# Performance work log

Hardware: AMD Instinct MI355X
Metric: run time of the kernel (lower is better)

## Reference

```python
import jax, jax.numpy as jnp
import numpy as np

E = 256        # HP.EMBED_SIZE
R = 8          # number of derivation rules / MLPs
S = 512        # number of sequential derivation steps
N = 256        # nodes produced per step
N_INIT = 1024  # initial axiom (thax) embeddings
TOTAL = N_INIT + S * N  # 132096 rows in the vectors buffer
M = 65536      # masked nodes fed to eval_net


def setup_inputs() -> dict:
    key = jax.random.key(0)
    ks = jax.random.split(key, 12)
    rng = np.random.default_rng(0)

    init_vecs = jax.random.normal(ks[0], (N_INIT, E), jnp.float32)
    # rule MLPs: concat(2 parents) -> E (relu) -> E
    W1 = jax.random.normal(ks[1], (R, 2 * E, E), jnp.float32) * (1.0 / np.sqrt(2 * E))
    b1 = jnp.zeros((R, E), jnp.float32)
    W2 = jax.random.normal(ks[2], (R, E, E), jnp.float32) * (1.0 / np.sqrt(E))
    b2 = jnp.zeros((R, E), jnp.float32)
    # eval net: E -> E (relu) -> 1
    eval_W1 = jax.random.normal(ks[3], (E, E), jnp.float32) * (1.0 / np.sqrt(E))
    eval_b1 = jnp.zeros((E,), jnp.float32)
    eval_W2 = jax.random.normal(ks[4], (E, 1), jnp.float32) * (1.0 / np.sqrt(E))
    eval_b2 = jnp.zeros((1,), jnp.float32)

    # step s writes rows [N_INIT + s*N, N_INIT + (s+1)*N)
    ind_steps = (N_INIT + np.arange(S * N, dtype=np.int32)).reshape(S, N)
    # parents drawn causally from already-computed prefix [0, N_INIT + s*N)
    highs = (N_INIT + np.arange(S, dtype=np.int64) * N)[:, None, None]
    pars_ind_steps = (rng.random((S, N, 2)) * highs).astype(np.int32)
    rule_steps = rng.integers(0, R, size=(S,)).astype(np.int32)
    mask = rng.integers(0, TOTAL, size=(M,)).astype(np.int32)

    pos = jax.random.uniform(ks[5], (M,), jnp.float32)
    neg = jax.random.uniform(ks[6], (M,), jnp.float32)
    target = jnp.round(jax.random.uniform(ks[7], (M,), jnp.float32))

    return {
        'init_vecs': init_vecs, 'W1': W1, 'b1': b1, 'W2': W2, 'b2': b2,
        'eval_W1': eval_W1, 'eval_b1': eval_b1, 'eval_W2': eval_W2, 'eval_b2': eval_b2,
        'pos': pos, 'neg': neg, 'target': target,
        'ind_steps': jnp.asarray(ind_steps), 'pars_ind_steps': jnp.asarray(pars_ind_steps),
        'rule_steps': jnp.asarray(rule_steps), 'mask': jnp.asarray(mask),
    }


def reference(init_vecs, W1, b1, W2, b2, eval_W1, eval_b1, eval_W2, eval_b2,
              pos, neg, target, ind_steps, pars_ind_steps, rule_steps, mask):
    vectors = jnp.zeros((TOTAL, E), init_vecs.dtype).at[:N_INIT].set(init_vecs)

    def step(vec, xs):
        inds, pars, r = xs            # [N], [N,2], scalar rule id
        p = vec[pars].reshape(N, 2 * E)   # gather parents
        h = jax.nn.relu(p @ W1[r] + b1[r])
        out = h @ W2[r] + b2[r]
        return vec.at[inds].set(out), None  # scatter new node embeddings

    vectors, _ = jax.lax.scan(step, vectors, (ind_steps, pars_ind_steps, rule_steps))

    x = vectors[mask]
    val = (jax.nn.relu(x @ eval_W1 + eval_b1) @ eval_W2 + eval_b2)[:, 0]

    # pos_weight = POS_WEIGHT_EXTRA * tot_neg / tot_pos (constant w.r.t. grads)
    pw = jax.lax.stop_gradient(jnp.sum(neg) / jnp.maximum(jnp.sum(pos), 1.0))
    # BCEWithLogitsLoss(pos_weight, reduction='none')
    contrib = pw * target * jax.nn.softplus(-val) + (1.0 - target) * jax.nn.softplus(val)
    loss = jnp.sum((pos + neg) * contrib)
    posOK = jnp.sum(pos * (val >= 0))
    negOK = jnp.sum(neg * (val < 0))
    return loss, posOK, negOK
```

## Files before the change

kernel.cpp:

```cpp
#include <hip/hip_runtime.h>
#include <math.h>

#define EMB   256
#define TWOE  512
#define NINIT 1024
#define NSTEP 512
#define NPS   256
#define TOTAL (NINIT + NSTEP * NPS)
#define MM    65536
#define NNODE (NSTEP * NPS)
#define NKEY  2048
#define BTH   512
#define TROWS 32
#define CHK_SH  16384
#define RULE_SH (24 * CHK_SH)

typedef short s16x8 __attribute__((ext_vector_type(8)));
typedef float f32x4 __attribute__((ext_vector_type(4)));

#define OFF_VECH   0ull
#define OFF_VECL   ((size_t)TOTAL * EMB * 2)
#define OFF_VAL    (2ull * (size_t)TOTAL * EMB * 2)
#define OFF_CNT    (OFF_VAL + (size_t)MM * 4)
#define OFF_ACC    (OFF_CNT + 4096)
#define OFF_PW     (OFF_ACC + 64)
#define OFF_KCNT   (OFF_PW + 192)
#define OFF_KOFS   (OFF_KCNT + (size_t)NKEY * 4)
#define OFF_NL     (OFF_KOFS + (size_t)NKEY * 4)
#define OFF_BROWS  (OFF_NL + 256)
#define OFF_LVL8   (OFF_BROWS + (size_t)NNODE * 4)
#define OFF_WSPLIT (OFF_LVL8 + 132352)


__device__ __forceinline__ void store_dev_u32(unsigned* p, unsigned v) {
  asm volatile("global_store_dword %0, %1, off sc0 sc1" :: "v"(p), "v"(v) : "memory");
}
__device__ __forceinline__ void store_dev_b64(void* p, uint2 v) {
  asm volatile("global_store_dwordx2 %0, %1, off sc0 sc1" :: "v"(p), "v"(v) : "memory");
}
__device__ __forceinline__ void store_dev_b128(void* p, uint4 v) {
  store_dev_b64(p, make_uint2(v.x, v.y));
  store_dev_b64((char*)p + 8, make_uint2(v.z, v.w));
}
__device__ __forceinline__ unsigned load_dev_u32(const unsigned* p) {
  unsigned r;
  asm volatile("global_load_dword %0, %1, off sc0 sc1\n\ts_waitcnt vmcnt(0)"
               : "=v"(r) : "v"(p) : "memory");
  return r;
}

__device__ __forceinline__ void gbar_full(unsigned* gc, unsigned* gep) {
  asm volatile("s_waitcnt vmcnt(0)" ::: "memory");
  __syncthreads();
  if (threadIdx.x == 0) {
    unsigned old = __hip_atomic_fetch_add(gc, 1u, __ATOMIC_RELAXED, __HIP_MEMORY_SCOPE_AGENT);
    unsigned tgt = old / 256u + 1u;
    if ((old & 255u) == 255u) store_dev_u32(gep, tgt);
    else while (load_dev_u32(gep) < tgt) __builtin_amdgcn_s_sleep(1);
  }
  __syncthreads();
}

__device__ __forceinline__ void split8(const float* f, uint4& h4, uint4& l4) {
  unsigned hu[8], lu[8];
  #pragma unroll
  for (int i = 0; i < 8; ++i) {
    unsigned u = __builtin_bit_cast(unsigned, f[i]);
    float rh = __builtin_bit_cast(float, u & 0xffff0000u);
    float rl = f[i] - rh;
    hu[i] = u >> 16;
    lu[i] = __builtin_bit_cast(unsigned, rl) >> 16;
  }
  h4 = make_uint4(hu[0] | (hu[1] << 16), hu[2] | (hu[3] << 16),
                  hu[4] | (hu[5] << 16), hu[6] | (hu[7] << 16));
  l4 = make_uint4(lu[0] | (lu[1] << 16), lu[2] | (lu[3] << 16),
                  lu[4] | (lu[5] << 16), lu[6] | (lu[7] << 16));
}

__global__ void zero_scratch(unsigned* cnt, double* acc) {
  for (int i = threadIdx.x; i < 1024; i += 256) cnt[i] = 0u;
  if (threadIdx.x < 8) acc[threadIdx.x] = 0.0;
}

__global__ void init_convert(const float* __restrict__ src,
                             unsigned short* __restrict__ vh,
                             unsigned short* __restrict__ vl) {
  int slot = blockIdx.x * blockDim.x + threadIdx.x;
  float f[8];
  *(float4*)&f[0] = reinterpret_cast<const float4*>(src)[slot * 2];
  *(float4*)&f[4] = reinterpret_cast<const float4*>(src)[slot * 2 + 1];
  uint4 h4, l4;
  split8(f, h4, l4);
  *(uint4*)(vh + (size_t)slot * 8) = h4;
  *(uint4*)(vl + (size_t)slot * 8) = l4;
}

__global__ __launch_bounds__(512)
void presplit(const float* __restrict__ W1, const float* __restrict__ W2,
              short* __restrict__ Ws)
{
  const int blk = blockIdx.x;
  const int r = blk / 24, c = blk % 24;
  const float* src; int kbase;
  if (c < 16) { src = W1 + (size_t)r * TWOE * EMB; kbase = c * 32; }
  else        { src = W2 + (size_t)r * EMB * EMB;  kbase = (c - 16) * 32; }
  short* dst = Ws + (size_t)blk * CHK_SH;
  const int tid = threadIdx.x;
  #pragma unroll
  for (int u = 0; u < 2; ++u) {
    int qq = tid + u * 512;
    int g = qq >> 6, l = qq & 63;
    const float* p = src + (size_t)(kbase + ((l >> 4) << 3)) * EMB + (g << 4) + (l & 15);
    float f[8];
    #pragma unroll
    for (int i = 0; i < 8; ++i) f[i] = p[i * EMB];
    uint4 h4, l4;
    split8(f, h4, l4);
    *(uint4*)(dst + (size_t)qq * 8) = h4;
    *(uint4*)(dst + 8192 + (size_t)qq * 8) = l4;
  }
}

__global__ __launch_bounds__(256)
void prepass_levels(const int* __restrict__ pars, unsigned char* __restrict__ lvl8,
                    int* __restrict__ nlp)
{
  __shared__ unsigned char slvl[TOTAL];
  __shared__ int swmax[4];
  const int t = threadIdx.x;
  for (int i = t; i < NINIT; i += 256) slvl[i] = 0;
  __syncthreads();
  int Pa[8], Pb[8];
  #pragma unroll
  for (int w = 0; w < 8; ++w) {
    Pa[w] = pars[2 * (w * NPS + t)];
    Pb[w] = pars[2 * (w * NPS + t) + 1];
  }
  int lmax = 0;
  for (int s0 = 0; s0 < NSTEP; s0 += 8) {
    int Na[8], Nb[8];
    if (s0 + 8 < NSTEP) {
      #pragma unroll
      for (int w = 0; w < 8; ++w) {
        Na[w] = pars[2 * ((s0 + 8 + w) * NPS + t)];
        Nb[w] = pars[2 * ((s0 + 8 + w) * NPS + t) + 1];
      }
    } else {
      #pragma unroll
      for (int w = 0; w < 8; ++w) { Na[w] = 0; Nb[w] = 0; }
    }
    #pragma unroll
    for (int w = 0; w < 8; ++w) {
      int l1 = slvl[Pa[w]], l2 = slvl[Pb[w]];
      int lv = 1 + (l1 > l2 ? l1 : l2);
      slvl[NINIT + (s0 + w) * NPS + t] = (unsigned char)lv;
      if (lv > lmax) lmax = lv;
      __syncthreads();
    }
    #pragma unroll
    for (int w = 0; w < 8; ++w) { Pa[w] = Na[w]; Pb[w] = Nb[w]; }
  }
  const unsigned* sv = (const unsigned*)slvl;
  unsigned* gv = (unsigned*)lvl8;
  for (int i = t; i < TOTAL / 4; i += 256) gv[i] = sv[i];
  for (int o = 32; o; o >>= 1) lmax = max(lmax, __shfl_down(lmax, o));
  if ((t & 63) == 0) swmax[t >> 6] = lmax;
  __syncthreads();
  if (t == 0) {
    int m = 0;
    for (int w = 0; w < 4; ++w) m = max(m, swmax[w]);
    nlp[0] = m;
  }
}

__global__ __launch_bounds__(1024)
void prepass_bucket(const unsigned char* __restrict__ lvl8, const int* __restrict__ rules,
                    int* __restrict__ kcnt, int* __restrict__ kofs,
                    int* __restrict__ brows)
{
  __shared__ int scnt[NKEY];
  __shared__ int sofs[NKEY];
  const int t = threadIdx.x;
  for (int k = t; k < NKEY; k += 1024) scnt[k] = 0;
  __syncthreads();
  for (int i = t; i < NNODE; i += 1024) {
    int key = (int)lvl8[NINIT + i] * 8 + rules[i >> 8];
    atomicAdd(&scnt[key], 1);
  }
  __syncthreads();
  if (t == 0) {
    int run = 0;
    for (int k = 0; k < NKEY; ++k) {
      sofs[k] = run; kofs[k] = run; kcnt[k] = scnt[k]; run += scnt[k];
    }
  }
  __syncthreads();
  for (int i = t; i < NNODE; i += 1024) {
    int key = (int)lvl8[NINIT + i] * 8 + rules[i >> 8];
    int pos = atomicAdd(&sofs[key], 1);
    brows[pos] = i;
  }
}

__global__ __launch_bounds__(BTH, 1)
void scan_kernel(const short* __restrict__ Ws, const float* __restrict__ b1,
                 const float* __restrict__ b2, const int* __restrict__ pars,
                 unsigned short* __restrict__ vech, unsigned short* __restrict__ vecl,
                 const int* __restrict__ kcnt, const int* __restrict__ kofs,
                 const int* __restrict__ brows, const int* __restrict__ nlp,
                 unsigned* __restrict__ cnt)
{
  __shared__ float hL[TROWS][260];
  __shared__ int spar[2 * TROWS];
  __shared__ int sorow[TROWS];
  const int tid = threadIdx.x;
  const int bid = blockIdx.x;
  const int lane = tid & 63;
  const int w = tid >> 6;
  const int rw = w & 1, cwb = (w >> 1) << 2;
  const int row16 = lane & 15, kb8 = (lane >> 4) << 3;
  const int arow = (rw << 4) + row16;
  unsigned* gc  = cnt;
  unsigned* gep = cnt + 32;
  const int NL = nlp[0];
  const int xcd = bid & 7, jb = bid >> 3;

  for (int lv = 1; lv <= NL; ++lv) {
    int cum[9]; cum[0] = 0;
    int cnts[8], ofss[8];
    #pragma unroll
    for (int r = 0; r < 8; ++r) {
      int c = kcnt[lv * 8 + r];
      cnts[r] = c; ofss[r] = kofs[lv * 8 + r];
      cum[r + 1] = cum[r] + ((c + TROWS - 1) >> 5);
    }
    const int G = cum[8];
    const int q = G >> 3, rm = G & 7;
    const int Gx = q + (xcd < rm ? 1 : 0);
    const int sx = xcd * q + (xcd < rm ? xcd : rm);
    for (int j = jb; j < Gx; j += 32) {
      const int g = sx + j;
      int rr = 0;
      while (g >= cum[rr + 1]) ++rr;
      const int t0 = g - cum[rr];
      const int cnt_b = cnts[rr], ofs_b = ofss[rr];
      const int tbase = t0 * TROWS;
      const short* __restrict__ Wr = Ws + (size_t)rr * RULE_SH;

      __syncthreads();
      if (tid < 2 * TROWS) {
        int slot = tbase + (tid >> 1);
        if (slot >= cnt_b) slot = cnt_b - 1;
        int node = brows[ofs_b + slot];
        spar[tid] = pars[2 * node + (tid & 1)];
        if ((tid & 1) == 0) sorow[tid >> 1] = NINIT + node;
      }
      __syncthreads();
      const int par0 = spar[2 * arow], par1 = spar[2 * arow + 1];
      float b1v[4];
      #pragma unroll
      for (int g4 = 0; g4 < 4; ++g4)
        b1v[g4] = b1[rr * EMB + ((cwb + g4) << 4) + row16];

      uint4 ahA, alA;
      {
        size_t off = (size_t)par0 * EMB + kb8;
        ahA = *(const uint4*)(vech + off);
        alA = *(const uint4*)(vecl + off);
      }
      f32x4 acc[4] = {{0,0,0,0},{0,0,0,0},{0,0,0,0},{0,0,0,0}};
      #pragma unroll 2
      for (int c = 0; c < 16; ++c) {
        uint4 ahB = ahA, alB = alA;
        if (c < 15) {
          int kglob = (c + 1) * 32 + kb8;
          int par = (kglob >> 8) ? par1 : par0;
          size_t off = (size_t)par * EMB + (kglob & 255);
          ahB = *(const uint4*)(vech + off);
          alB = *(const uint4*)(vecl + off);
        }
        const short* ch = Wr + (size_t)c * CHK_SH;
        s16x8 Ah = __builtin_bit_cast(s16x8, ahA);
        s16x8 Al = __builtin_bit_cast(s16x8, alA);
        #pragma unroll
        for (int g4 = 0; g4 < 4; ++g4) {
          int gi = (cwb + g4) * 64 + lane;
          s16x8 Bh = *(const s16x8*)(ch + (size_t)gi * 8);
          s16x8 Bl = *(const s16x8*)(ch + 8192 + (size_t)gi * 8);
          acc[g4] = __builtin_amdgcn_mfma_f32_16x16x32_bf16(Ah, Bh, acc[g4], 0, 0, 0);
          acc[g4] = __builtin_amdgcn_mfma_f32_16x16x32_bf16(Ah, Bl, acc[g4], 0, 0, 0);
          acc[g4] = __builtin_amdgcn_mfma_f32_16x16x32_bf16(Al, Bh, acc[g4], 0, 0, 0);
        }
        ahA = ahB; alA = alB;
      }
      #pragma unroll
      for (int g4 = 0; g4 < 4; ++g4) {
        #pragma unroll
        for (int jj = 0; jj < 4; ++jj)
          hL[(rw << 4) + ((lane >> 4) << 2) + jj][((cwb + g4) << 4) + row16] =
              fmaxf(acc[g4][jj] + b1v[g4], 0.f);
      }
      __syncthreads();
      float b2v[4];
      #pragma unroll
      for (int g4 = 0; g4 < 4; ++g4)
        b2v[g4] = b2[rr * EMB + ((cwb + g4) << 4) + row16];
      f32x4 acc2[4] = {{0,0,0,0},{0,0,0,0},{0,0,0,0},{0,0,0,0}};
      for (int c2 = 0; c2 < 8; ++c2) {
        const short* ch = Wr + (size_t)(16 + c2) * CHK_SH;
        uint4 a2h, a2l;
        {
          float af[8];
          *(float4*)&af[0] = *(const float4*)&hL[arow][c2 * 32 + kb8];
          *(float4*)&af[4] = *(const float4*)&hL[arow][c2 * 32 + kb8 + 4];
          split8(af, a2h, a2l);
        }
        s16x8 Ah = __builtin_bit_cast(s16x8, a2h);
        s16x8 Al = __builtin_bit_cast(s16x8, a2l);
        #pragma unroll
        for (int g4 = 0; g4 < 4; ++g4) {
          int gi = (cwb + g4) * 64 + lane;
          s16x8 Bh = *(const s16x8*)(ch + (size_t)gi * 8);
          s16x8 Bl = *(const s16x8*)(ch + 8192 + (size_t)gi * 8);
          acc2[g4] = __builtin_amdgcn_mfma_f32_16x16x32_bf16(Ah, Bh, acc2[g4], 0, 0, 0);
          acc2[g4] = __builtin_amdgcn_mfma_f32_16x16x32_bf16(Ah, Bl, acc2[g4], 0, 0, 0);
          acc2[g4] = __builtin_amdgcn_mfma_f32_16x16x32_bf16(Al, Bh, acc2[g4], 0, 0, 0);
        }
      }
      __syncthreads();
      #pragma unroll
      for (int g4 = 0; g4 < 4; ++g4) {
        #pragma unroll
        for (int jj = 0; jj < 4; ++jj)
          hL[(rw << 4) + ((lane >> 4) << 2) + jj][((cwb + g4) << 4) + row16] =
              acc2[g4][jj] + b2v[g4];
      }
      __syncthreads();
      #pragma unroll
      for (int u = 0; u < 2; ++u) {
        int s = tid + u * 512;
        int row = s >> 5, c8 = (s & 31) * 8;
        float of[8];
        *(float4*)&of[0] = *(const float4*)&hL[row][c8];
        *(float4*)&of[4] = *(const float4*)&hL[row][c8 + 4];
        uint4 h4, l4;
        split8(of, h4, l4);
        if (tbase + row < cnt_b) {
          size_t off = (size_t)sorow[row] * EMB + c8;
          store_dev_b128(vech + off, h4);
          store_dev_b128(vecl + off, l4);
        }
      }
    }
    gbar_full(gc, gep);
  }
}

__global__ void reduce_pn(const float* __restrict__ pos, const float* __restrict__ neg,
                          double* acc) {
  double sp = 0.0, sn = 0.0;
  for (int m = blockIdx.x * blockDim.x + threadIdx.x; m < MM; m += gridDim.x * blockDim.x) {
    sp += (double)pos[m]; sn += (double)neg[m];
  }
  for (int o = 32; o; o >>= 1) { sp += __shfl_down(sp, o); sn += __shfl_down(sn, o); }
  __shared__ double rp[4], rn[4];
  int wid = threadIdx.x >> 6, lane = threadIdx.x & 63;
  if (lane == 0) { rp[wid] = sp; rn[wid] = sn; }
  __syncthreads();
  if (threadIdx.x == 0) {
    double tp = 0.0, tn = 0.0;
    for (int w = 0; w < 4; ++w) { tp += rp[w]; tn += rn[w]; }
    atomicAdd(&acc[0], tp); atomicAdd(&acc[1], tn);
  }
}

__global__ void pw_kernel(const double* __restrict__ acc, float* __restrict__ pw) {
  pw[0] = (float)(acc[1] / fmax(acc[0], 1.0));
}

__global__ __launch_bounds__(256)
void eval_kernel(const unsigned short* __restrict__ vh, const unsigned short* __restrict__ vl,
                 const int* __restrict__ mask,
                 const float* __restrict__ eW1, const float* __restrict__ eb1,
                 const float* __restrict__ eW2, const float* __restrict__ eb2,
                 float* __restrict__ val)
{
  __shared__ float xL[64][36];
  __shared__ float wLx[32][260];
  __shared__ int mrow[64];
  const int tid = threadIdx.x;
  const int a = tid >> 4, b = tid & 15;
  const int m0 = blockIdx.x * 64;
  if (tid < 64) mrow[tid] = mask[m0 + tid];
  __syncthreads();

  float acc[4][16];
  #pragma unroll
  for (int i = 0; i < 4; ++i)
    #pragma unroll
    for (int j = 0; j < 16; ++j) acc[i][j] = 0.f;

  for (int c = 0; c < 8; ++c) {
    const int e0 = c * 32;
    for (int idx = tid; idx < 64 * 4; idx += 256) {
      int rr = idx >> 2, u = idx & 3;
      size_t off = (size_t)mrow[rr] * EMB + e0 + u * 8;
      uint4 hv = *(const uint4*)(vh + off);
      uint4 lv = *(const uint4*)(vl + off);
      const unsigned* hu = (const unsigned*)&hv;
      const unsigned* lu = (const unsigned*)&lv;
      float fo[8];
      #pragma unroll
      for (int jj = 0; jj < 4; ++jj) {
        fo[2 * jj] = __builtin_bit_cast(float, (hu[jj] & 0xffffu) << 16) +
                     __builtin_bit_cast(float, (lu[jj] & 0xffffu) << 16);
        fo[2 * jj + 1] = __builtin_bit_cast(float, hu[jj] & 0xffff0000u) +
                         __builtin_bit_cast(float, lu[jj] & 0xffff0000u);
      }
      *(float4*)&xL[rr][u * 8] = *(float4*)&fo[0];
      *(float4*)&xL[rr][u * 8 + 4] = *(float4*)&fo[4];
    }
    for (int idx = tid; idx < 32 * 64; idx += 256) {
      int e = idx >> 6, k4 = idx & 63;
      reinterpret_cast<float4*>(&wLx[e][0])[k4] =
          reinterpret_cast<const float4*>(eW1 + (size_t)(e0 + e) * EMB)[k4];
    }
    __syncthreads();
    #pragma unroll 4
    for (int e = 0; e < 32; ++e) {
      float xs[4];
      #pragma unroll
      for (int rr = 0; rr < 4; ++rr) xs[rr] = xL[a * 4 + rr][e];
      const float4* wr = reinterpret_cast<const float4*>(&wLx[e][0]) + b * 4;
      float wk[16];
      *reinterpret_cast<float4*>(&wk[0])  = wr[0];
      *reinterpret_cast<float4*>(&wk[4])  = wr[1];
      *reinterpret_cast<float4*>(&wk[8])  = wr[2];
      *reinterpret_cast<float4*>(&wk[12]) = wr[3];
      #pragma unroll
      for (int rr = 0; rr < 4; ++rr)
        #pragma unroll
        for (int kk = 0; kk < 16; ++kk)
          acc[rr][kk] = fmaf(xs[rr], wk[kk], acc[rr][kk]);
    }
    __syncthreads();
  }

  float eb2v = eb2[0];
  float pv[4];
  #pragma unroll
  for (int rr = 0; rr < 4; ++rr) {
    float s = 0.f;
    #pragma unroll
    for (int kk = 0; kk < 16; ++kk) {
      float h = acc[rr][kk] + eb1[b * 16 + kk];
      h = fmaxf(h, 0.f);
      s += h * eW2[b * 16 + kk];
    }
    pv[rr] = s;
  }
  #pragma unroll
  for (int m = 1; m < 16; m <<= 1) {
    #pragma unroll
    for (int rr = 0; rr < 4; ++rr) pv[rr] += __shfl_xor(pv[rr], m);
  }
  if (b == 0) {
    #pragma unroll
    for (int rr = 0; rr < 4; ++rr) val[m0 + a * 4 + rr] = pv[rr] + eb2v;
  }
}

__global__ void loss_kernel(const float* __restrict__ val, const float* __restrict__ pos,
                            const float* __restrict__ neg, const float* __restrict__ tgt,
                            const float* __restrict__ pwp, double* acc)
{
  const float pw = pwp[0];
  double l = 0.0, pk = 0.0, nk = 0.0;
  for (int m = blockIdx.x * blockDim.x + threadIdx.x; m < MM; m += gridDim.x * blockDim.x) {
    float v = val[m], p = pos[m], n = neg[m], t = tgt[m];
    float lp = log1pf(expf(-fabsf(v)));
    float spn = fmaxf(-v, 0.f) + lp;
    float spp = fmaxf(v, 0.f) + lp;
    float contrib = pw * t * spn + (1.f - t) * spp;
    l += (double)((p + n) * contrib);
    if (v >= 0.f) pk += (double)p; else nk += (double)n;
  }
  for (int o = 32; o; o >>= 1) {
    l += __shfl_down(l, o); pk += __shfl_down(pk, o); nk += __shfl_down(nk, o);
  }
  __shared__ double s0[4], s1[4], s2[4];
  int wid = threadIdx.x >> 6, lane = threadIdx.x & 63;
  if (lane == 0) { s0[wid] = l; s1[wid] = pk; s2[wid] = nk; }
  __syncthreads();
  if (threadIdx.x == 0) {
    double ta = 0.0, tb = 0.0, tc = 0.0;
    for (int w = 0; w < 4; ++w) { ta += s0[w]; tb += s1[w]; tc += s2[w]; }
    atomicAdd(&acc[2], ta); atomicAdd(&acc[3], tb); atomicAdd(&acc[4], tc);
  }
}

__global__ void writeout(const double* __restrict__ acc, float* __restrict__ out) {
  if (threadIdx.x == 0) {
    out[0] = (float)acc[2];
    out[1] = (float)acc[3];
    out[2] = (float)acc[4];
  }
}

extern "C" void kernel_launch(void* const* d_in, const int* in_sizes, int n_in,
                              void* d_out, int out_size, void* d_ws, size_t ws_size,
                              hipStream_t stream)
{
  (void)in_sizes; (void)n_in; (void)out_size; (void)ws_size;
  const float* init_vecs = (const float*)d_in[0];
  const float* W1  = (const float*)d_in[1];
  const float* b1  = (const float*)d_in[2];
  const float* W2  = (const float*)d_in[3];
  const float* b2  = (const float*)d_in[4];
  const float* eW1 = (const float*)d_in[5];
  const float* eb1 = (const float*)d_in[6];
  const float* eW2 = (const float*)d_in[7];
  const float* eb2 = (const float*)d_in[8];
  const float* pos = (const float*)d_in[9];
  const float* neg = (const float*)d_in[10];
  const float* tgt = (const float*)d_in[11];
  const int* pars  = (const int*)d_in[13];
  const int* rules = (const int*)d_in[14];
  const int* mask  = (const int*)d_in[15];

  char* ws = (char*)d_ws;
  unsigned short* vech = (unsigned short*)(ws + OFF_VECH);
  unsigned short* vecl = (unsigned short*)(ws + OFF_VECL);
  float*    val   = (float*)(ws + OFF_VAL);
  unsigned* cnt   = (unsigned*)(ws + OFF_CNT);
  double*   acc   = (double*)(ws + OFF_ACC);
  float*    pw    = (float*)(ws + OFF_PW);
  int*      kcnt  = (int*)(ws + OFF_KCNT);
  int*      kofs  = (int*)(ws + OFF_KOFS);
  int*      nlp   = (int*)(ws + OFF_NL);
  int*      brows = (int*)(ws + OFF_BROWS);
  unsigned char* lvl8 = (unsigned char*)(ws + OFF_LVL8);
  short*    Ws    = (short*)(ws + OFF_WSPLIT);

  zero_scratch<<<1, 256, 0, stream>>>(cnt, acc);
  prepass_levels<<<1, 256, 0, stream>>>(pars, lvl8, nlp);
  prepass_bucket<<<1, 1024, 0, stream>>>(lvl8, rules, kcnt, kofs, brows);
  init_convert<<<128, 256, 0, stream>>>(init_vecs, vech, vecl);
  presplit<<<192, 512, 0, stream>>>(W1, W2, Ws);
  scan_kernel<<<256, BTH, 0, stream>>>(Ws, b1, b2, pars, vech, vecl,
                                       kcnt, kofs, brows, nlp, cnt);
  reduce_pn<<<128, 256, 0, stream>>>(pos, neg, acc);
  pw_kernel<<<1, 1, 0, stream>>>(acc, pw);
  eval_kernel<<<1024, 256, 0, stream>>>(vech, vecl, mask, eW1, eb1, eW2, eb2, val);
  loss_kernel<<<128, 256, 0, stream>>>(val, pos, neg, tgt, pw, acc);
  writeout<<<1, 1, 0, stream>>>(acc, (float*)d_out);
}
```

Measured before the change: 1.323 ms.

## Software-pipeline parent and weight loads in scan MLP, use hierarchical grid barrier

Replaces the single flat grid barrier with a two-level tree barrier. Each XCD group of 32 blocks counts on its own counter, and only the last arriver touches a global counter, which cuts atomic contention between levels. The MLP inner loops now prefetch parent rows four chunks ahead and double-buffer the weight fragments and the layer-2 A split one chunk ahead, so global loads overlap the MFMA work. This raises register pressure, and the counter layout assumes the cnt buffer has at least 608 words zeroed.

```diff
diff --git a/kernel.cpp b/kernel.cpp
--- a/kernel.cpp
+++ b/kernel.cpp
@@ -49,14 +49,25 @@
   return r;
 }
 
-__device__ __forceinline__ void gbar_full(unsigned* gc, unsigned* gep) {
+__device__ __forceinline__ void gbar_tree(unsigned* cnt, int xcd) {
   asm volatile("s_waitcnt vmcnt(0)" ::: "memory");
   __syncthreads();
   if (threadIdx.x == 0) {
-    unsigned old = __hip_atomic_fetch_add(gc, 1u, __ATOMIC_RELAXED, __HIP_MEMORY_SCOPE_AGENT);
-    unsigned tgt = old / 256u + 1u;
-    if ((old & 255u) == 255u) store_dev_u32(gep, tgt);
-    else while (load_dev_u32(gep) < tgt) __builtin_amdgcn_s_sleep(1);
+    unsigned* xarr = cnt + 32 * xcd;
+    unsigned* garr = cnt + 512;
+    unsigned* gep  = cnt + 544;
+    unsigned* xep  = cnt + 576 + 32 * xcd;
+    unsigned o = __hip_atomic_fetch_add(xarr, 1u, __ATOMIC_RELAXED, __HIP_MEMORY_SCOPE_AGENT);
+    unsigned tgt = o / 32u + 1u;
+    if ((o & 31u) == 31u) {
+      unsigned g = __hip_atomic_fetch_add(garr, 1u, __ATOMIC_RELAXED, __HIP_MEMORY_SCOPE_AGENT);
+      unsigned gt = g / 8u + 1u;
+      if ((g & 7u) == 7u) store_dev_u32(gep, gt);
+      else while (load_dev_u32(gep) < gt) __builtin_amdgcn_s_sleep(1);
+      store_dev_u32(xep, tgt);
+    } else {
+      while (load_dev_u32(xep) < tgt) __builtin_amdgcn_s_sleep(1);
+    }
   }
   __syncthreads();
 }
@@ -220,8 +231,6 @@
   const int rw = w & 1, cwb = (w >> 1) << 2;
   const int row16 = lane & 15, kb8 = (lane >> 4) << 3;
   const int arow = (rw << 4) + row16;
-  unsigned* gc  = cnt;
-  unsigned* gep = cnt + 32;
   const int NL = nlp[0];
   const int xcd = bid & 7, jb = bid >> 3;
 
@@ -257,41 +266,65 @@
       }
       __syncthreads();
       const int par0 = spar[2 * arow], par1 = spar[2 * arow + 1];
-      float b1v[4];
-      #pragma unroll
-      for (int g4 = 0; g4 < 4; ++g4)
+      float b1v[4], b2v[4];
+      #pragma unroll
+      for (int g4 = 0; g4 < 4; ++g4) {
         b1v[g4] = b1[rr * EMB + ((cwb + g4) << 4) + row16];
-
-      uint4 ahA, alA;
+        b2v[g4] = b2[rr * EMB + ((cwb + g4) << 4) + row16];
+      }
+
+      uint4 pAh[4], pAl[4];
+      #pragma unroll
+      for (int d = 0; d < 4; ++d) {
+        size_t off = (size_t)par0 * EMB + d * 32 + kb8;
+        pAh[d] = *(const uint4*)(vech + off);
+        pAl[d] = *(const uint4*)(vecl + off);
+      }
+      uint4 pBh[2][4], pBl[2][4];
+      #pragma unroll
+      for (int g4 = 0; g4 < 4; ++g4) {
+        int gi = (cwb + g4) * 64 + lane;
+        pBh[0][g4] = *(const uint4*)(Wr + (size_t)gi * 8);
+        pBl[0][g4] = *(const uint4*)(Wr + 8192 + (size_t)gi * 8);
+      }
+      f32x4 acc[4] = {{0,0,0,0},{0,0,0,0},{0,0,0,0},{0,0,0,0}};
+      #pragma unroll
+      for (int c = 0; c < 16; ++c) {
+        s16x8 AhC = __builtin_bit_cast(s16x8, pAh[c & 3]);
+        s16x8 AlC = __builtin_bit_cast(s16x8, pAl[c & 3]);
+        if (c + 4 < 16) {
+          int kg = (c + 4) * 32 + kb8;
+          int par = (kg >> 8) ? par1 : par0;
+          size_t off = (size_t)par * EMB + (kg & 255);
+          pAh[c & 3] = *(const uint4*)(vech + off);
+          pAl[c & 3] = *(const uint4*)(vecl + off);
+        }
+        if (c + 1 < 16) {
+          const short* chn = Wr + (size_t)(c + 1) * CHK_SH;
+          #pragma unroll
+          for (int g4 = 0; g4 < 4; ++g4) {
+            int gi = (cwb + g4) * 64 + lane;
+            pBh[(c + 1) & 1][g4] = *(const uint4*)(chn + (size_t)gi * 8);
+            pBl[(c + 1) & 1][g4] = *(const uint4*)(chn + 8192 + (size_t)gi * 8);
+          }
+        }
+        #pragma unroll
+        for (int g4 = 0; g4 < 4; ++g4) {
+          s16x8 Bh = __builtin_bit_cast(s16x8, pBh[c & 1][g4]);
+          s16x8 Bl = __builtin_bit_cast(s16x8, pBl[c & 1][g4]);
+          acc[g4] = __builtin_amdgcn_mfma_f32_16x16x32_bf16(AhC, Bh, acc[g4], 0, 0, 0);
+          acc[g4] = __builtin_amdgcn_mfma_f32_16x16x32_bf16(AhC, Bl, acc[g4], 0, 0, 0);
+          acc[g4] = __builtin_amdgcn_mfma_f32_16x16x32_bf16(AlC, Bh, acc[g4], 0, 0, 0);
+        }
+      }
       {
-        size_t off = (size_t)par0 * EMB + kb8;
-        ahA = *(const uint4*)(vech + off);
-        alA = *(const uint4*)(vecl + off);
-      }
-      f32x4 acc[4] = {{0,0,0,0},{0,0,0,0},{0,0,0,0},{0,0,0,0}};
-      #pragma unroll 2
-      for (int c = 0; c < 16; ++c) {
-        uint4 ahB = ahA, alB = alA;
-        if (c < 15) {
-          int kglob = (c + 1) * 32 + kb8;
-          int par = (kglob >> 8) ? par1 : par0;
-          size_t off = (size_t)par * EMB + (kglob & 255);
-          ahB = *(const uint4*)(vech + off);
-          alB = *(const uint4*)(vecl + off);
-        }
-        const short* ch = Wr + (size_t)c * CHK_SH;
-        s16x8 Ah = __builtin_bit_cast(s16x8, ahA);
-        s16x8 Al = __builtin_bit_cast(s16x8, alA);
+        const short* chn = Wr + (size_t)16 * CHK_SH;
         #pragma unroll
         for (int g4 = 0; g4 < 4; ++g4) {
           int gi = (cwb + g4) * 64 + lane;
-          s16x8 Bh = *(const s16x8*)(ch + (size_t)gi * 8);
-          s16x8 Bl = *(const s16x8*)(ch + 8192 + (size_t)gi * 8);
-          acc[g4] = __builtin_amdgcn_mfma_f32_16x16x32_bf16(Ah, Bh, acc[g4], 0, 0, 0);
-          acc[g4] = __builtin_amdgcn_mfma_f32_16x16x32_bf16(Ah, Bl, acc[g4], 0, 0, 0);
-          acc[g4] = __builtin_amdgcn_mfma_f32_16x16x32_bf16(Al, Bh, acc[g4], 0, 0, 0);
-        }
-        ahA = ahB; alA = alB;
+          pBh[0][g4] = *(const uint4*)(chn + (size_t)gi * 8);
+          pBl[0][g4] = *(const uint4*)(chn + 8192 + (size_t)gi * 8);
+        }
       }
       #pragma unroll
       for (int g4 = 0; g4 < 4; ++g4) {
@@ -301,30 +334,38 @@
               fmaxf(acc[g4][jj] + b1v[g4], 0.f);
       }
       __syncthreads();
-      float b2v[4];
-      #pragma unroll
-      for (int g4 = 0; g4 < 4; ++g4)
-        b2v[g4] = b2[rr * EMB + ((cwb + g4) << 4) + row16];
+      uint4 qh[2], ql[2];
+      {
+        float af[8];
+        *(float4*)&af[0] = *(const float4*)&hL[arow][kb8];
+        *(float4*)&af[4] = *(const float4*)&hL[arow][kb8 + 4];
+        split8(af, qh[0], ql[0]);
+      }
       f32x4 acc2[4] = {{0,0,0,0},{0,0,0,0},{0,0,0,0},{0,0,0,0}};
+      #pragma unroll
       for (int c2 = 0; c2 < 8; ++c2) {
-        const short* ch = Wr + (size_t)(16 + c2) * CHK_SH;
-        uint4 a2h, a2l;
-        {
+        s16x8 AhC = __builtin_bit_cast(s16x8, qh[c2 & 1]);
+        s16x8 AlC = __builtin_bit_cast(s16x8, ql[c2 & 1]);
+        if (c2 + 1 < 8) {
           float af[8];
-          *(float4*)&af[0] = *(const float4*)&hL[arow][c2 * 32 + kb8];
-          *(float4*)&af[4] = *(const float4*)&hL[arow][c2 * 32 + kb8 + 4];
-          split8(af, a2h, a2l);
-        }
-        s16x8 Ah = __builtin_bit_cast(s16x8, a2h);
-        s16x8 Al = __builtin_bit_cast(s16x8, a2l);
+          *(float4*)&af[0] = *(const float4*)&hL[arow][(c2 + 1) * 32 + kb8];
+          *(float4*)&af[4] = *(const float4*)&hL[arow][(c2 + 1) * 32 + kb8 + 4];
+          split8(af, qh[(c2 + 1) & 1], ql[(c2 + 1) & 1]);
+          const short* chn = Wr + (size_t)(17 + c2) * CHK_SH;
+          #pragma unroll
+          for (int g4 = 0; g4 < 4; ++g4) {
+            int gi = (cwb + g4) * 64 + lane;
+            pBh[(c2 + 1) & 1][g4] = *(const uint4*)(chn + (size_t)gi * 8);
+            pBl[(c2 + 1) & 1][g4] = *(const uint4*)(chn + 8192 + (size_t)gi * 8);
+          }
+        }
         #pragma unroll
         for (int g4 = 0; g4 < 4; ++g4) {
-          int gi = (cwb + g4) * 64 + lane;
-          s16x8 Bh = *(const s16x8*)(ch + (size_t)gi * 8);
-          s16x8 Bl = *(const s16x8*)(ch + 8192 + (size_t)gi * 8);
-          acc2[g4] = __builtin_amdgcn_mfma_f32_16x16x32_bf16(Ah, Bh, acc2[g4], 0, 0, 0);
-          acc2[g4] = __builtin_amdgcn_mfma_f32_16x16x32_bf16(Ah, Bl, acc2[g4], 0, 0, 0);
-          acc2[g4] = __builtin_amdgcn_mfma_f32_16x16x32_bf16(Al, Bh, acc2[g4], 0, 0, 0);
+          s16x8 Bh = __builtin_bit_cast(s16x8, pBh[c2 & 1][g4]);
+          s16x8 Bl = __builtin_bit_cast(s16x8, pBl[c2 & 1][g4]);
+          acc2[g4] = __builtin_amdgcn_mfma_f32_16x16x32_bf16(AhC, Bh, acc2[g4], 0, 0, 0);
+          acc2[g4] = __builtin_amdgcn_mfma_f32_16x16x32_bf16(AhC, Bl, acc2[g4], 0, 0, 0);
+          acc2[g4] = __builtin_amdgcn_mfma_f32_16x16x32_bf16(AlC, Bh, acc2[g4], 0, 0, 0);
         }
       }
       __syncthreads();
@@ -352,7 +393,7 @@
         }
       }
     }
-    gbar_full(gc, gep);
+    gbar_tree(cnt, xcd);
   }
 }
 
```

Measured after the change: 1.280 ms. 3.3% less time.

## Split row tiles across 4-block clusters with LDS weight ring and per-level counters

Applied to the files above, without the earlier changes.

Replaces the full-grid barrier per dependency level with per-level completion counters, so each level only waits until the previous level's tiles are done. Tiles grow to 64 rows and are processed by clusters of 4 blocks that each own a 64-column slice. The hidden activations are exchanged through a global buffer behind a small cluster barrier. Weight chunks are streamed into a 6-slot LDS ring with global_load_lds and explicit vmcnt waits, and activation loads are prefetched two chunks ahead. This aims to cut global barrier cost and weight reload bandwidth, at the price of extra cluster syncs, a global round trip for the hidden layer, and delicate hand-written wait counts.

```diff
diff --git a/kernel.cpp b/kernel.cpp
--- a/kernel.cpp
+++ b/kernel.cpp
@@ -11,7 +11,7 @@
 #define NNODE (NSTEP * NPS)
 #define NKEY  2048
 #define BTH   512
-#define TROWS 32
+#define TROWS 64
 #define CHK_SH  16384
 #define RULE_SH (24 * CHK_SH)
 
@@ -22,14 +22,16 @@
 #define OFF_VECL   ((size_t)TOTAL * EMB * 2)
 #define OFF_VAL    (2ull * (size_t)TOTAL * EMB * 2)
 #define OFF_CNT    (OFF_VAL + (size_t)MM * 4)
-#define OFF_ACC    (OFF_CNT + 4096)
+#define OFF_ACC    (OFF_CNT + 32768)
 #define OFF_PW     (OFF_ACC + 64)
 #define OFF_KCNT   (OFF_PW + 192)
 #define OFF_KOFS   (OFF_KCNT + (size_t)NKEY * 4)
 #define OFF_NL     (OFF_KOFS + (size_t)NKEY * 4)
 #define OFF_BROWS  (OFF_NL + 256)
 #define OFF_LVL8   (OFF_BROWS + (size_t)NNODE * 4)
-#define OFF_WSPLIT (OFF_LVL8 + 132352)
+#define OFF_TPL    (OFF_LVL8 + 132352)
+#define OFF_HB     (OFF_TPL + 4096)
+#define OFF_WSPLIT (OFF_HB + 4194304)
 
 
 __device__ __forceinline__ void store_dev_u32(unsigned* p, unsigned v) {
@@ -48,17 +50,22 @@
                : "=v"(r) : "v"(p) : "memory");
   return r;
 }
-
-__device__ __forceinline__ void gbar_full(unsigned* gc, unsigned* gep) {
-  asm volatile("s_waitcnt vmcnt(0)" ::: "memory");
-  __syncthreads();
-  if (threadIdx.x == 0) {
-    unsigned old = __hip_atomic_fetch_add(gc, 1u, __ATOMIC_RELAXED, __HIP_MEMORY_SCOPE_AGENT);
-    unsigned tgt = old / 256u + 1u;
-    if ((old & 255u) == 255u) store_dev_u32(gep, tgt);
-    else while (load_dev_u32(gep) < tgt) __builtin_amdgcn_s_sleep(1);
-  }
-  __syncthreads();
+__device__ __forceinline__ uint4 load_coh_b128(const void* p) {
+  uint4 r;
+  asm volatile("global_load_dwordx4 %0, %1, off sc0 sc1" : "=v"(r) : "v"(p) : "memory");
+  return r;
+}
+__device__ __forceinline__ void wait_vm(int n) {
+  switch (n) {
+    case 0:  asm volatile("s_waitcnt vmcnt(0)"  ::: "memory"); break;
+    case 1:  asm volatile("s_waitcnt vmcnt(1)"  ::: "memory"); break;
+    case 2:  asm volatile("s_waitcnt vmcnt(2)"  ::: "memory"); break;
+    case 3:  asm volatile("s_waitcnt vmcnt(3)"  ::: "memory"); break;
+    case 7:  asm volatile("s_waitcnt vmcnt(7)"  ::: "memory"); break;
+    case 9:  asm volatile("s_waitcnt vmcnt(9)"  ::: "memory"); break;
+    case 11: asm volatile("s_waitcnt vmcnt(11)" ::: "memory"); break;
+    default: asm volatile("s_waitcnt vmcnt(13)" ::: "memory"); break;
+  }
 }
 
 __device__ __forceinline__ void split8(const float* f, uint4& h4, uint4& l4) {
@@ -76,10 +83,28 @@
   l4 = make_uint4(lu[0] | (lu[1] << 16), lu[2] | (lu[3] << 16),
                   lu[4] | (lu[5] << 16), lu[6] | (lu[7] << 16));
 }
+__device__ __forceinline__ void split1(float f, short& hi, short& lo) {
+  unsigned u = __builtin_bit_cast(unsigned, f);
+  float rh = __builtin_bit_cast(float, u & 0xffff0000u);
+  float rl = f - rh;
+  hi = (short)(u >> 16);
+  lo = (short)(__builtin_bit_cast(unsigned, rl) >> 16);
+}
+
+__device__ __forceinline__ void stage_slice(short* dstbase, const short* Wr, int chunk,
+                                            int q, int w, int lane) {
+  const short* src = Wr + (size_t)chunk * CHK_SH + ((w >> 2) ? 8192 : 0)
+                   + (((q << 2) + (w & 3)) * 64 + lane) * 8;
+  short* dst = dstbase + ((w >> 2) ? 2048 : 0) + ((w & 3) * 64 + lane) * 8;
+  __builtin_amdgcn_global_load_lds(
+      (const __attribute__((address_space(1))) unsigned int*)src,
+      (__attribute__((address_space(3))) unsigned int*)dst, 16, 0, 0);
+}
 
 __global__ void zero_scratch(unsigned* cnt, double* acc) {
-  for (int i = threadIdx.x; i < 1024; i += 256) cnt[i] = 0u;
-  if (threadIdx.x < 8) acc[threadIdx.x] = 0.0;
+  int i = blockIdx.x * 256 + threadIdx.x;
+  if (i < 8192) cnt[i] = 0u;
+  if (i < 8) acc[i] = 0.0;
 }
 
 __global__ void init_convert(const float* __restrict__ src,
@@ -176,7 +201,7 @@
 __global__ __launch_bounds__(1024)
 void prepass_bucket(const unsigned char* __restrict__ lvl8, const int* __restrict__ rules,
                     int* __restrict__ kcnt, int* __restrict__ kofs,
-                    int* __restrict__ brows)
+                    int* __restrict__ brows, int* __restrict__ tpl)
 {
   __shared__ int scnt[NKEY];
   __shared__ int sofs[NKEY];
@@ -194,6 +219,12 @@
       sofs[k] = run; kofs[k] = run; kcnt[k] = scnt[k]; run += scnt[k];
     }
   }
+  if (t < 256) {
+    int s = 0;
+    #pragma unroll
+    for (int r = 0; r < 8; ++r) s += (scnt[t * 8 + r] + TROWS - 1) >> 6;
+    tpl[t] = s;
+  }
   __syncthreads();
   for (int i = t; i < NNODE; i += 1024) {
     int key = (int)lvl8[NINIT + i] * 8 + rules[i >> 8];
@@ -207,152 +238,195 @@
                  const float* __restrict__ b2, const int* __restrict__ pars,
                  unsigned short* __restrict__ vech, unsigned short* __restrict__ vecl,
                  const int* __restrict__ kcnt, const int* __restrict__ kofs,
-                 const int* __restrict__ brows, const int* __restrict__ nlp,
-                 unsigned* __restrict__ cnt)
+                 const int* __restrict__ brows, const int* __restrict__ tpl,
+                 const int* __restrict__ nlp, unsigned* __restrict__ cnt,
+                 unsigned short* __restrict__ hb)
 {
-  __shared__ float hL[TROWS][260];
+  __shared__ short ring[6][4096];
+  __shared__ short hH[TROWS][264];
+  __shared__ short hLo[TROWS][264];
   __shared__ int spar[2 * TROWS];
   __shared__ int sorow[TROWS];
   const int tid = threadIdx.x;
   const int bid = blockIdx.x;
   const int lane = tid & 63;
   const int w = tid >> 6;
-  const int rw = w & 1, cwb = (w >> 1) << 2;
+  const int rw2 = w & 3;
+  const int cg = w >> 2;
   const int row16 = lane & 15, kb8 = (lane >> 4) << 3;
-  const int arow = (rw << 4) + row16;
-  unsigned* gc  = cnt;
-  unsigned* gep = cnt + 32;
+  const int arow = (rw2 << 4) + row16;
+  const int hrow0 = (rw2 << 4) + ((lane >> 4) << 2);
+  const int ct = bid >> 2;
+  const int q = bid & 3;
+  unsigned* done = cnt;
+  unsigned* ccnt = cnt + 256 + ct * 32;
+  unsigned* cep  = cnt + 2304 + ct * 32;
+  unsigned short* hbh = hb + (size_t)ct * 32768;
+  unsigned short* hbl = hbh + 16384;
   const int NL = nlp[0];
-  const int xcd = bid & 7, jb = bid >> 3;
 
   for (int lv = 1; lv <= NL; ++lv) {
+    if (tid == 0 && lv > 1) {
+      const unsigned need = 4u * (unsigned)tpl[lv - 1];
+      while (load_dev_u32(done + (lv - 1)) < need) __builtin_amdgcn_s_sleep(2);
+    }
+    __syncthreads();
     int cum[9]; cum[0] = 0;
     int cnts[8], ofss[8];
     #pragma unroll
     for (int r = 0; r < 8; ++r) {
       int c = kcnt[lv * 8 + r];
       cnts[r] = c; ofss[r] = kofs[lv * 8 + r];
-      cum[r + 1] = cum[r] + ((c + TROWS - 1) >> 5);
+      cum[r + 1] = cum[r] + ((c + TROWS - 1) >> 6);
     }
     const int G = cum[8];
-    const int q = G >> 3, rm = G & 7;
-    const int Gx = q + (xcd < rm ? 1 : 0);
-    const int sx = xcd * q + (xcd < rm ? xcd : rm);
-    for (int j = jb; j < Gx; j += 32) {
-      const int g = sx + j;
+    for (int j = ct; j < G; j += 64) {
       int rr = 0;
-      while (g >= cum[rr + 1]) ++rr;
-      const int t0 = g - cum[rr];
-      const int cnt_b = cnts[rr], ofs_b = ofss[rr];
-      const int tbase = t0 * TROWS;
+      while (j >= cum[rr + 1]) ++rr;
+      const int t0 = j - cum[rr];
+      const int cb = min(TROWS, cnts[rr] - t0 * TROWS);
+      const int ofs = ofss[rr] + t0 * TROWS;
       const short* __restrict__ Wr = Ws + (size_t)rr * RULE_SH;
 
-      __syncthreads();
       if (tid < 2 * TROWS) {
-        int slot = tbase + (tid >> 1);
-        if (slot >= cnt_b) slot = cnt_b - 1;
-        int node = brows[ofs_b + slot];
+        int sl = tid >> 1;
+        if (sl >= cb) sl = cb - 1;
+        int node = brows[ofs + sl];
         spar[tid] = pars[2 * node + (tid & 1)];
         if ((tid & 1) == 0) sorow[tid >> 1] = NINIT + node;
       }
       __syncthreads();
-      const int par0 = spar[2 * arow], par1 = spar[2 * arow + 1];
-      float b1v[4];
-      #pragma unroll
-      for (int g4 = 0; g4 < 4; ++g4)
-        b1v[g4] = b1[rr * EMB + ((cwb + g4) << 4) + row16];
-
-      uint4 ahA, alA;
-      {
-        size_t off = (size_t)par0 * EMB + kb8;
-        ahA = *(const uint4*)(vech + off);
-        alA = *(const uint4*)(vecl + off);
-      }
-      f32x4 acc[4] = {{0,0,0,0},{0,0,0,0},{0,0,0,0},{0,0,0,0}};
-      #pragma unroll 2
+      const int p0 = spar[2 * arow], p1 = spar[2 * arow + 1];
+      float b1v[2], b2v[2];
+      int colg_[2];
+      #pragma unroll
+      for (int g4 = 0; g4 < 2; ++g4) {
+        int gl = (cg << 1) + g4;
+        colg_[g4] = (q << 6) + (gl << 4) + row16;
+        b1v[g4] = b1[rr * EMB + colg_[g4]];
+        b2v[g4] = b2[rr * EMB + colg_[g4]];
+      }
+      stage_slice(&ring[0][0], Wr, 0, q, w, lane);
+      stage_slice(&ring[1][0], Wr, 1, q, w, lane);
+      stage_slice(&ring[2][0], Wr, 2, q, w, lane);
+      stage_slice(&ring[3][0], Wr, 3, q, w, lane);
+      uint4 aH[3], aL[3];
+      #define LOAD_A(c_, s_) { int kg = (c_) * 32 + kb8; \
+        int par = (kg >> 8) ? p1 : p0; \
+        size_t off = (size_t)par * EMB + (kg & 255); \
+        aH[s_] = *(const uint4*)(vech + off); aL[s_] = *(const uint4*)(vecl + off); }
+      LOAD_A(0, 0); LOAD_A(1, 1);
+      f32x4 acc[2] = {{0,0,0,0},{0,0,0,0}};
+      #pragma unroll
       for (int c = 0; c < 16; ++c) {
-        uint4 ahB = ahA, alB = alA;
-        if (c < 15) {
-          int kglob = (c + 1) * 32 + kb8;
-          int par = (kglob >> 8) ? par1 : par0;
-          size_t off = (size_t)par * EMB + (kglob & 255);
-          ahB = *(const uint4*)(vech + off);
-          alB = *(const uint4*)(vecl + off);
-        }
-        const short* ch = Wr + (size_t)c * CHK_SH;
-        s16x8 Ah = __builtin_bit_cast(s16x8, ahA);
-        s16x8 Al = __builtin_bit_cast(s16x8, alA);
+        wait_vm(c == 0 ? 7 : c == 1 ? 9 : c == 2 ? 11 : c == 3 ? 13 : c == 15 ? 9 : 11);
+        __builtin_amdgcn_s_barrier();
+        const short* rs = &ring[c % 6][0];
+        s16x8 Ah = __builtin_bit_cast(s16x8, aH[c % 3]);
+        s16x8 Al = __builtin_bit_cast(s16x8, aL[c % 3]);
         #pragma unroll
-        for (int g4 = 0; g4 < 4; ++g4) {
-          int gi = (cwb + g4) * 64 + lane;
-          s16x8 Bh = *(const s16x8*)(ch + (size_t)gi * 8);
-          s16x8 Bl = *(const s16x8*)(ch + 8192 + (size_t)gi * 8);
+        for (int g4 = 0; g4 < 2; ++g4) {
+          int gl = (cg << 1) + g4;
+          s16x8 Bh = *(const s16x8*)(rs + ((gl * 64 + lane) << 3));
+          s16x8 Bl = *(const s16x8*)(rs + 2048 + ((gl * 64 + lane) << 3));
           acc[g4] = __builtin_amdgcn_mfma_f32_16x16x32_bf16(Ah, Bh, acc[g4], 0, 0, 0);
           acc[g4] = __builtin_amdgcn_mfma_f32_16x16x32_bf16(Ah, Bl, acc[g4], 0, 0, 0);
           acc[g4] = __builtin_amdgcn_mfma_f32_16x16x32_bf16(Al, Bh, acc[g4], 0, 0, 0);
         }
-        ahA = ahB; alA = alB;
-      }
-      #pragma unroll
-      for (int g4 = 0; g4 < 4; ++g4) {
+        if (c + 4 <= 19) stage_slice(&ring[(c + 4) % 6][0], Wr, c + 4, q, w, lane);
+        if (c + 2 <= 15) LOAD_A(c + 2, (c + 2) % 3);
+      }
+      #pragma unroll
+      for (int g4 = 0; g4 < 2; ++g4) {
         #pragma unroll
-        for (int jj = 0; jj < 4; ++jj)
-          hL[(rw << 4) + ((lane >> 4) << 2) + jj][((cwb + g4) << 4) + row16] =
-              fmaxf(acc[g4][jj] + b1v[g4], 0.f);
-      }
-      __syncthreads();
-      float b2v[4];
-      #pragma unroll
-      for (int g4 = 0; g4 < 4; ++g4)
-        b2v[g4] = b2[rr * EMB + ((cwb + g4) << 4) + row16];
-      f32x4 acc2[4] = {{0,0,0,0},{0,0,0,0},{0,0,0,0},{0,0,0,0}};
-      for (int c2 = 0; c2 < 8; ++c2) {
-        const short* ch = Wr + (size_t)(16 + c2) * CHK_SH;
-        uint4 a2h, a2l;
-        {
-          float af[8];
-          *(float4*)&af[0] = *(const float4*)&hL[arow][c2 * 32 + kb8];
-          *(float4*)&af[4] = *(const float4*)&hL[arow][c2 * 32 + kb8 + 4];
-          split8(af, a2h, a2l);
+        for (int jj = 0; jj < 4; ++jj) {
+          short hi, lo;
+          split1(fmaxf(acc[g4][jj] + b1v[g4], 0.f), hi, lo);
+          hH[hrow0 + jj][colg_[g4]] = hi;
+          hLo[hrow0 + jj][colg_[g4]] = lo;
         }
-        s16x8 Ah = __builtin_bit_cast(s16x8, a2h);
-        s16x8 Al = __builtin_bit_cast(s16x8, a2l);
+      }
+      __syncthreads();
+      {
+        int row = tid >> 3, jj = tid & 7;
+        int cg8 = (q << 6) + jj * 8;
+        store_dev_b128(hbh + row * 256 + cg8, *(const uint4*)&hH[row][cg8]);
+        store_dev_b128(hbl + row * 256 + cg8, *(const uint4*)&hLo[row][cg8]);
+      }
+      __syncthreads();
+      if (tid == 0) {
+        unsigned old = __hip_atomic_fetch_add(ccnt, 1u, __ATOMIC_RELAXED,
+                                              __HIP_MEMORY_SCOPE_AGENT);
+        unsigned tgt = old / 4u + 1u;
+        if ((old & 3u) == 3u) store_dev_u32(cep, tgt);
+        else while (load_dev_u32(cep) < tgt) __builtin_amdgcn_s_sleep(1);
+      }
+      __syncthreads();
+      {
+        uint4 rh[4], rl[4];
         #pragma unroll
-        for (int g4 = 0; g4 < 4; ++g4) {
-          int gi = (cwb + g4) * 64 + lane;
-          s16x8 Bh = *(const s16x8*)(ch + (size_t)gi * 8);
-          s16x8 Bl = *(const s16x8*)(ch + 8192 + (size_t)gi * 8);
+        for (int i = 0; i < 4; ++i) {
+          int idx = tid + i * 512;
+          int row = idx >> 5, jj = idx & 31;
+          rh[i] = load_coh_b128(hbh + row * 256 + jj * 8);
+          rl[i] = load_coh_b128(hbl + row * 256 + jj * 8);
+        }
+        asm volatile("s_waitcnt vmcnt(0)" ::: "memory");
+        __builtin_amdgcn_sched_barrier(0);
+        #pragma unroll
+        for (int i = 0; i < 4; ++i) {
+          int idx = tid + i * 512;
+          int row = idx >> 5, jj = idx & 31;
+          *(uint4*)&hH[row][jj * 8] = rh[i];
+          *(uint4*)&hLo[row][jj * 8] = rl[i];
+        }
+      }
+      __syncthreads();
+      f32x4 acc2[2] = {{0,0,0,0},{0,0,0,0}};
+      #pragma unroll
+      for (int c2 = 16; c2 < 24; ++c2) {
+        if (c2 >= 20) wait_vm(23 - c2);
+        __builtin_amdgcn_s_barrier();
+        const short* rs = &ring[c2 % 6][0];
+        const int kc = ((c2 - 16) << 5) + kb8;
+        s16x8 Ah = *(const s16x8*)&hH[arow][kc];
+        s16x8 Al = *(const s16x8*)&hLo[arow][kc];
+        #pragma unroll
+        for (int g4 = 0; g4 < 2; ++g4) {
+          int gl = (cg << 1) + g4;
+          s16x8 Bh = *(const s16x8*)(rs + ((gl * 64 + lane) << 3));
+          s16x8 Bl = *(const s16x8*)(rs + 2048 + ((gl * 64 + lane) << 3));
           acc2[g4] = __builtin_amdgcn_mfma_f32_16x16x32_bf16(Ah, Bh, acc2[g4], 0, 0, 0);
           acc2[g4] = __builtin_amdgcn_mfma_f32_16x16x32_bf16(Ah, Bl, acc2[g4], 0, 0, 0);
           acc2[g4] = __builtin_amdgcn_mfma_f32_16x16x32_bf16(Al, Bh, acc2[g4], 0, 0, 0);
         }
-      }
-      __syncthreads();
-      #pragma unroll
-      for (int g4 = 0; g4 < 4; ++g4) {
+        if (c2 + 4 <= 23) stage_slice(&ring[(c2 + 4) % 6][0], Wr, c2 + 4, q, w, lane);
+      }
+      __syncthreads();
+      #pragma unroll
+      for (int g4 = 0; g4 < 2; ++g4) {
         #pragma unroll
-        for (int jj = 0; jj < 4; ++jj)
-          hL[(rw << 4) + ((lane >> 4) << 2) + jj][((cwb + g4) << 4) + row16] =
-              acc2[g4][jj] + b2v[g4];
-      }
-      __syncthreads();
-      #pragma unroll
-      for (int u = 0; u < 2; ++u) {
-        int s = tid + u * 512;
-        int row = s >> 5, c8 = (s & 31) * 8;
-        float of[8];
-        *(float4*)&of[0] = *(const float4*)&hL[row][c8];
-        *(float4*)&of[4] = *(const float4*)&hL[row][c8 + 4];
-        uint4 h4, l4;
-        split8(of, h4, l4);
-        if (tbase + row < cnt_b) {
-          size_t off = (size_t)sorow[row] * EMB + c8;
-          store_dev_b128(vech + off, h4);
-          store_dev_b128(vecl + off, l4);
+        for (int jj = 0; jj < 4; ++jj) {
+          short hi, lo;
+          split1(acc2[g4][jj] + b2v[g4], hi, lo);
+          hH[hrow0 + jj][colg_[g4]] = hi;
+          hLo[hrow0 + jj][colg_[g4]] = lo;
         }
       }
-    }
-    gbar_full(gc, gep);
+      __syncthreads();
+      {
+        int row = tid >> 3, jj = tid & 7;
+        int cg8 = (q << 6) + jj * 8;
+        if (row < cb) {
+          size_t off = (size_t)sorow[row] * EMB + cg8;
+          store_dev_b128(vech + off, *(const uint4*)&hH[row][cg8]);
+          store_dev_b128(vecl + off, *(const uint4*)&hLo[row][cg8]);
+        }
+      }
+      __syncthreads();
+      if (tid == 0)
+        __hip_atomic_fetch_add(done + lv, 1u, __ATOMIC_RELAXED, __HIP_MEMORY_SCOPE_AGENT);
+    }
   }
 }
 
@@ -540,15 +614,17 @@
   int*      nlp   = (int*)(ws + OFF_NL);
   int*      brows = (int*)(ws + OFF_BROWS);
   unsigned char* lvl8 = (unsigned char*)(ws + OFF_LVL8);
+  int*      tpl   = (int*)(ws + OFF_TPL);
+  unsigned short* hb = (unsigned short*)(ws + OFF_HB);
   short*    Ws    = (short*)(ws + OFF_WSPLIT);
 
-  zero_scratch<<<1, 256, 0, stream>>>(cnt, acc);
+  zero_scratch<<<32, 256, 0, stream>>>(cnt, acc);
   prepass_levels<<<1, 256, 0, stream>>>(pars, lvl8, nlp);
-  prepass_bucket<<<1, 1024, 0, stream>>>(lvl8, rules, kcnt, kofs, brows);
+  prepass_bucket<<<1, 1024, 0, stream>>>(lvl8, rules, kcnt, kofs, brows, tpl);
   init_convert<<<128, 256, 0, stream>>>(init_vecs, vech, vecl);
   presplit<<<192, 512, 0, stream>>>(W1, W2, Ws);
   scan_kernel<<<256, BTH, 0, stream>>>(Ws, b1, b2, pars, vech, vecl,
-                                       kcnt, kofs, brows, nlp, cnt);
+                                       kcnt, kofs, brows, tpl, nlp, cnt, hb);
   reduce_pn<<<128, 256, 0, stream>>>(pos, neg, acc);
   pw_kernel<<<1, 1, 0, stream>>>(acc, pw);
   eval_kernel<<<1024, 256, 0, stream>>>(vech, vecl, mask, eW1, eb1, eW2, eb2, val);
```

Result: slower. 1.457 ms (+10.1%).
